# Performance work log

Hardware: AMD Instinct MI355X
Metric: run time of the kernel (lower is better)

The kernel has to match this reference:

```python
import jax, jax.numpy as jnp
import numpy as np

N = 20000      # nodes
E = 320000     # edges (before self-loops)
C_IN, C_HID, C_OUT = 256, 256, 128
NEG_SLOPE = 0.2  # PyG GATConv default


def setup_inputs() -> dict:
    key = jax.random.key(0)
    ks = jax.random.split(key, 10)
    x = jax.random.normal(ks[0], (N, C_IN), dtype=jnp.float32)
    edge_index = jax.random.randint(ks[1], (2, E), 0, N, dtype=jnp.int64)

    def glorot(k, shape, fan):
        return jax.random.normal(k, shape, dtype=jnp.float32) / np.float32(np.sqrt(fan))

    W1 = glorot(ks[2], (C_IN, C_HID), C_IN)
    a_src1 = glorot(ks[3], (C_HID,), C_HID)
    a_dst1 = glorot(ks[4], (C_HID,), C_HID)
    b1 = jnp.zeros((C_HID,), jnp.float32)
    W2 = glorot(ks[5], (C_HID, C_OUT), C_HID)
    a_src2 = glorot(ks[6], (C_OUT,), C_OUT)
    a_dst2 = glorot(ks[7], (C_OUT,), C_OUT)
    b2 = jnp.zeros((C_OUT,), jnp.float32)
    return dict(x=x, edge_index=edge_index, W1=W1, a_src1=a_src1, a_dst1=a_dst1,
                b1=b1, W2=W2, a_src2=a_src2, a_dst2=a_dst2, b2=b2)


def gat_layer(x, src, dst, W, a_src, a_dst, b, n):
    # PyG GATConv (heads=1): linear proj, additive attention, softmax over
    # incoming edges per destination node, weighted aggregation + bias.
    h = x @ W                                   # [N, F]
    alpha_src = h @ a_src                       # [N]
    alpha_dst = h @ a_dst                       # [N]
    e = jax.nn.leaky_relu(alpha_src[src] + alpha_dst[dst], NEG_SLOPE)  # [E]
    m = jax.ops.segment_max(e, dst, num_segments=n)                    # stable softmax
    e = jnp.exp(e - m[dst])
    denom = jax.ops.segment_sum(e, dst, num_segments=n)                # [N]
    out = jax.ops.segment_sum(e[:, None] * h[src], dst, num_segments=n)  # [N, F]
    return out / denom[:, None] + b


def reference(x, edge_index, W1, a_src1, a_dst1, b1, W2, a_src2, a_dst2, b2):
    n = x.shape[0]
    # GATConv adds self-loops by default
    loops = jnp.arange(n, dtype=edge_index.dtype)
    ei = jnp.concatenate([edge_index, jnp.stack([loops, loops])], axis=1)
    src, dst = ei[0], ei[1]
    h = gat_layer(x, src, dst, W1, a_src1, a_dst1, b1, n)
    h = jax.nn.relu(h)  # Dropout is identity in eval mode
    return gat_layer(h, src, dst, W2, a_src2, a_dst2, b2, n)
```

## Files before the change

### kernel.cpp

```cpp
#include <hip/hip_runtime.h>
#include <math.h>

#define N_NODES 20000
#define N_EDGES 320000
#define C_IN  256
#define C_HID 256
#define C_OUT 128
#define NEG_SLOPE 0.2f
#define CAP   256
#define GEMM1_BLKS (N_NODES / 32)
#define SCAT_BLKS  ((N_EDGES + 255) / 256)
#define AGG_PAD 280

typedef __attribute__((ext_vector_type(8))) short bf16x8;
typedef __attribute__((ext_vector_type(4))) float f32x4;

__device__ __align__(16) unsigned short c_W1h[C_IN * C_HID], c_W1l[C_IN * C_HID];
__device__ __align__(16) unsigned short c_W2h[C_HID * C_OUT], c_W2l[C_HID * C_OUT];
__device__ float c_as1f[C_HID], c_ad1f[C_HID], c_b1f[C_HID];
__device__ float c_as2f[C_OUT], c_ad2f[C_OUT], c_b2f[C_OUT];
__device__ __align__(16) unsigned short g_h1b[(size_t)N_NODES * C_HID];
__device__ __align__(16) unsigned short g_h2b[(size_t)N_NODES * C_OUT];
__device__ float g_alps1[N_NODES], g_alpd1[N_NODES];
__device__ float g_alps2[N_NODES], g_alpd2[N_NODES];
__device__ int   g_cursor[N_NODES];
__device__ int   g_srcidx[(size_t)N_NODES * CAP];
__device__ int   g_is64;
__device__ int   g_isf32;

__device__ __forceinline__ float bf2f(unsigned short b){
  unsigned int u = ((unsigned int)b) << 16;
  return __builtin_bit_cast(float, u);
}
__device__ __forceinline__ unsigned short f2bf(float f){
  unsigned int u = __builtin_bit_cast(unsigned int, f);
  u += 0x7fffu + ((u >> 16) & 1u);
  return (unsigned short)(u >> 16);
}
__device__ __forceinline__ int clampi(int v){
  v = v < 0 ? 0 : v;
  return v >= N_NODES ? N_NODES - 1 : v;
}
__device__ __forceinline__ void edge_sd(const int* ei, int e, int& s, int& d){
  if (g_is64){ s = ei[2 * e]; d = ei[2 * (N_EDGES + e)]; }
  else       { s = ei[e];     d = ei[N_EDGES + e]; }
  s = clampi(s); d = clampi(d);
}

struct Ptrs { const void* p[8]; };

__device__ __forceinline__ int wpack(int k, int n, int Nc){
  return (((k >> 5) * (Nc / 16) + (n >> 4)) * 64 + (((k >> 3) & 3) * 16 + (n & 15))) * 8 + (k & 7);
}

#define PREP_Z  N_NODES
#define PREP_W1 (C_IN * C_HID)
#define PREP_W2 (C_HID * C_OUT)
#define PREP_T  (PREP_Z + PREP_W1 + PREP_W2 + 2 * C_HID + C_HID + 2 * C_OUT + C_OUT)

__global__ void prep_k(const unsigned int* __restrict__ xw,
                       const int* __restrict__ ei, Ptrs ps){
  __shared__ int s_isf32;
  if (threadIdx.x < 64){
    int lane = (int)threadIdx.x, cnt = 0;
    for (int j = lane; j < 256; j += 64){
      unsigned int e = (xw[j] >> 7) & 0xFFu;
      if (e >= 0x60u && e <= 0x8Fu) ++cnt;
    }
#pragma unroll
    for (int o = 32; o > 0; o >>= 1) cnt += __shfl_xor(cnt, o, 64);
    if (lane == 0) s_isf32 = (cnt < 200) ? 1 : 0;
  }
  __syncthreads();
  const int isf32 = s_isf32;

  if (blockIdx.x == 0 && threadIdx.x < 64){
    unsigned long long anybad = __ballot(ei[2 * (int)threadIdx.x + 1] != 0);
    if (threadIdx.x == 0){ g_isf32 = isf32; g_is64 = (anybad == 0ULL) ? 1 : 0; }
  }

  int tid = (int)(blockIdx.x * blockDim.x + threadIdx.x);
  if (tid < PREP_Z){
    g_cursor[tid] = 0;
    g_alps1[tid] = 0.f; g_alpd1[tid] = 0.f;
    g_alps2[tid] = 0.f; g_alpd2[tid] = 0.f;
    return;
  }
  int j = tid - PREP_Z;
  auto ld = [&](const void* p, int i) -> float {
    return isf32 ? ((const float*)p)[i] : bf2f(((const unsigned short*)p)[i]);
  };
  if (j < PREP_W1){
    float f = ld(ps.p[0], j);
    int k = j / C_HID, n = j % C_HID;
    int idx = wpack(k, n, C_HID);
    unsigned short h = f2bf(f);
    c_W1h[idx] = h; c_W1l[idx] = f2bf(f - bf2f(h));
    return;
  }
  j -= PREP_W1;
  if (j < PREP_W2){
    float f = ld(ps.p[4], j);
    int k = j / C_OUT, n = j % C_OUT;
    int idx = wpack(k, n, C_OUT);
    unsigned short h = f2bf(f);
    c_W2h[idx] = h; c_W2l[idx] = f2bf(f - bf2f(h));
    return;
  }
  j -= PREP_W2;
  if      (j <  256) c_as1f[j]        = ld(ps.p[1], j);
  else if (j <  512) c_ad1f[j - 256]  = ld(ps.p[2], j - 256);
  else if (j <  768) c_b1f [j - 512]  = ld(ps.p[3], j - 512);
  else if (j <  896) c_as2f[j - 768]  = ld(ps.p[5], j - 768);
  else if (j < 1024) c_ad2f[j - 896]  = ld(ps.p[6], j - 896);
  else if (j < 1152) c_b2f [j - 1024] = ld(ps.p[7], j - 1024);
}

__global__ __launch_bounds__(256) void gemm1_k(const void* __restrict__ xsrc,
                                               const int* __restrict__ ei){
  if (blockIdx.x >= GEMM1_BLKS){
    int e = (int)(blockIdx.x - GEMM1_BLKS) * 256 + (int)threadIdx.x;
    if (e < N_EDGES){
      int s, d;
      edge_sd(ei, e, s, d);
      int pos = atomicAdd(&g_cursor[d], 1);
      if (pos < CAP) g_srcidx[(size_t)d * CAP + pos] = s;
    }
    return;
  }

  const bool isf32 = (g_isf32 != 0);
  int wid  = (int)(threadIdx.x >> 6);
  int lane = (int)(threadIdx.x & 63);
  int kgrp = lane >> 4, cl = lane & 15;
  int mbase = blockIdx.x * 32;

  f32x4 acc[2][4];
#pragma unroll
  for (int m = 0; m < 2; ++m)
#pragma unroll
    for (int n = 0; n < 4; ++n) acc[m][n] = (f32x4){0.f, 0.f, 0.f, 0.f};

  for (int kt = 0; kt < 8; ++kt){
    int kbase = kt * 32 + kgrp * 8;
    bf16x8 ah[2], al[2];
    if (isf32){
      const float* Xf = (const float*)xsrc;
#pragma unroll
      for (int m = 0; m < 2; ++m){
        const float4* xp = (const float4*)(Xf + (size_t)(mbase + m * 16 + cl) * 256 + kbase);
        float4 v0 = xp[0], v1 = xp[1];
        float vals[8] = {v0.x, v0.y, v0.z, v0.w, v1.x, v1.y, v1.z, v1.w};
#pragma unroll
        for (int j = 0; j < 8; ++j){
          unsigned short h = f2bf(vals[j]);
          ah[m][j] = (short)h;
          al[m][j] = (short)f2bf(vals[j] - bf2f(h));
        }
      }
    } else {
      const unsigned short* Xb = (const unsigned short*)xsrc;
#pragma unroll
      for (int m = 0; m < 2; ++m){
        ah[m] = *(const bf16x8*)(Xb + (size_t)(mbase + m * 16 + cl) * 256 + kbase);
        al[m] = (bf16x8){0,0,0,0,0,0,0,0};
      }
    }
#pragma unroll
    for (int nn = 0; nn < 4; ++nn){
      int nt = wid * 4 + nn;
      size_t wi = ((size_t)(kt * 16 + nt) * 64 + lane) * 8;
      bf16x8 bh = *(const bf16x8*)(c_W1h + wi);
      bf16x8 bl = *(const bf16x8*)(c_W1l + wi);
#pragma unroll
      for (int m = 0; m < 2; ++m){
        acc[m][nn] = __builtin_amdgcn_mfma_f32_16x16x32_bf16(ah[m], bh, acc[m][nn], 0, 0, 0);
        acc[m][nn] = __builtin_amdgcn_mfma_f32_16x16x32_bf16(ah[m], bl, acc[m][nn], 0, 0, 0);
        acc[m][nn] = __builtin_amdgcn_mfma_f32_16x16x32_bf16(al[m], bh, acc[m][nn], 0, 0, 0);
      }
    }
  }

  float asv[4], adv[4];
#pragma unroll
  for (int nn = 0; nn < 4; ++nn){
    int col = (wid * 4 + nn) * 16 + cl;
    asv[nn] = c_as1f[col]; adv[nn] = c_ad1f[col];
  }
#pragma unroll
  for (int m = 0; m < 2; ++m){
#pragma unroll
    for (int i = 0; i < 4; ++i){
      int row = mbase + m * 16 + kgrp * 4 + i;
      float ps = 0.f, pd = 0.f;
#pragma unroll
      for (int nn = 0; nn < 4; ++nn){
        int col = (wid * 4 + nn) * 16 + cl;
        float v = acc[m][nn][i];
        g_h1b[(size_t)row * C_HID + col] = f2bf(v);
        ps += v * asv[nn]; pd += v * adv[nn];
      }
      ps += __shfl_xor(ps, 1);  pd += __shfl_xor(pd, 1);
      ps += __shfl_xor(ps, 2);  pd += __shfl_xor(pd, 2);
      ps += __shfl_xor(ps, 4);  pd += __shfl_xor(pd, 4);
      ps += __shfl_xor(ps, 8);  pd += __shfl_xor(pd, 8);
      if (cl == 0){
        atomicAdd(&g_alps1[row], ps);
        atomicAdd(&g_alpd1[row], pd);
      }
    }
  }
}

#define ACC4(p, ww) { \
  a0 += (ww) * bf2f((unsigned short)((p).x & 0xFFFFu)); \
  a1 += (ww) * bf2f((unsigned short)((p).x >> 16)); \
  a2 += (ww) * bf2f((unsigned short)((p).y & 0xFFFFu)); \
  a3 += (ww) * bf2f((unsigned short)((p).y >> 16)); }

#define ACC2(p, ww) { \
  a0 += (ww) * bf2f((unsigned short)((p) & 0xFFFFu)); \
  a1 += (ww) * bf2f((unsigned short)((p) >> 16)); }

__global__ __launch_bounds__(256) void aggemm_k(){
  __shared__ __align__(16) unsigned short s_hi[16 * AGG_PAD];
  __shared__ __align__(16) unsigned short s_lo[16 * AGG_PAD];
  __shared__ float s_ps[4][16], s_pd[4][16];

  int lane = (int)(threadIdx.x & 63);
  int wid  = (int)(threadIdx.x >> 6);
  int nb   = blockIdx.x * 16;
  const uint2* H2 = (const uint2*)g_h1b;

  for (int q = 0; q < 4; ++q){
    int n = nb + wid * 4 + q;
    int len = g_cursor[n]; if (len > CAP) len = CAP;
    int i0 = n * CAP, i1 = i0 + len;
    float adn = g_alpd1[n];
    float dpart = 0.f;
    float a0 = 0.f, a1 = 0.f, a2 = 0.f, a3 = 0.f;

    {
      float es = g_alps1[n] + adn;
      es = (es > 0.f) ? es : NEG_SLOPE * es;
      float wself = __expf(es);
      if (lane == 0) dpart += wself;
      uint2 p = H2[(size_t)n * 64 + lane];
      ACC4(p, wself)
    }

    for (int base = i0; base < i1; base += 64){
      int nv = i1 - base; if (nv > 64) nv = 64;
      int sv = 0; float wv = 0.f;
      if (lane < nv){
        sv = g_srcidx[base + lane];
        float e = g_alps1[sv] + adn;
        e = (e > 0.f) ? e : NEG_SLOPE * e;
        wv = __expf(e);
      }
      dpart += wv;
      int j = 0;
      for (; j + 8 <= nv; j += 8){
        int s0 = __shfl(sv, j),     s1 = __shfl(sv, j + 1);
        int s2 = __shfl(sv, j + 2), s3 = __shfl(sv, j + 3);
        int s4 = __shfl(sv, j + 4), s5 = __shfl(sv, j + 5);
        int s6 = __shfl(sv, j + 6), s7 = __shfl(sv, j + 7);
        float w0 = __shfl(wv, j),     w1 = __shfl(wv, j + 1);
        float w2 = __shfl(wv, j + 2), w3 = __shfl(wv, j + 3);
        float w4 = __shfl(wv, j + 4), w5 = __shfl(wv, j + 5);
        float w6 = __shfl(wv, j + 6), w7 = __shfl(wv, j + 7);
        uint2 p0 = H2[(size_t)s0 * 64 + lane];
        uint2 p1 = H2[(size_t)s1 * 64 + lane];
        uint2 p2 = H2[(size_t)s2 * 64 + lane];
        uint2 p3 = H2[(size_t)s3 * 64 + lane];
        uint2 p4 = H2[(size_t)s4 * 64 + lane];
        uint2 p5 = H2[(size_t)s5 * 64 + lane];
        uint2 p6 = H2[(size_t)s6 * 64 + lane];
        uint2 p7 = H2[(size_t)s7 * 64 + lane];
        ACC4(p0, w0) ACC4(p1, w1) ACC4(p2, w2) ACC4(p3, w3)
        ACC4(p4, w4) ACC4(p5, w5) ACC4(p6, w6) ACC4(p7, w7)
      }
      for (; j + 4 <= nv; j += 4){
        int s0 = __shfl(sv, j),     s1 = __shfl(sv, j + 1);
        int s2 = __shfl(sv, j + 2), s3 = __shfl(sv, j + 3);
        float w0 = __shfl(wv, j),     w1 = __shfl(wv, j + 1);
        float w2 = __shfl(wv, j + 2), w3 = __shfl(wv, j + 3);
        uint2 p0 = H2[(size_t)s0 * 64 + lane];
        uint2 p1 = H2[(size_t)s1 * 64 + lane];
        uint2 p2 = H2[(size_t)s2 * 64 + lane];
        uint2 p3 = H2[(size_t)s3 * 64 + lane];
        ACC4(p0, w0) ACC4(p1, w1) ACC4(p2, w2) ACC4(p3, w3)
      }
      for (; j < nv; ++j){
        int s = __shfl(sv, j);
        float w = __shfl(wv, j);
        uint2 p = H2[(size_t)s * 64 + lane];
        ACC4(p, w)
      }
    }

    float den = dpart;
#pragma unroll
    for (int o = 32; o > 0; o >>= 1) den += __shfl_xor(den, o, 64);
    float inv = 1.f / den;

    float o0 = a0 * inv + c_b1f[4 * lane];
    float o1 = a1 * inv + c_b1f[4 * lane + 1];
    float o2 = a2 * inv + c_b1f[4 * lane + 2];
    float o3 = a3 * inv + c_b1f[4 * lane + 3];
    o0 = fmaxf(o0, 0.f); o1 = fmaxf(o1, 0.f);
    o2 = fmaxf(o2, 0.f); o3 = fmaxf(o3, 0.f);
    unsigned short h0 = f2bf(o0), h1 = f2bf(o1), h2 = f2bf(o2), h3 = f2bf(o3);
    uint2 ph, pl;
    ph.x = (unsigned)h0 | ((unsigned)h1 << 16);
    ph.y = (unsigned)h2 | ((unsigned)h3 << 16);
    pl.x = (unsigned)f2bf(o0 - bf2f(h0)) | ((unsigned)f2bf(o1 - bf2f(h1)) << 16);
    pl.y = (unsigned)f2bf(o2 - bf2f(h2)) | ((unsigned)f2bf(o3 - bf2f(h3)) << 16);
    int r = wid * 4 + q;
    *(uint2*)&s_hi[r * AGG_PAD + 4 * lane] = ph;
    *(uint2*)&s_lo[r * AGG_PAD + 4 * lane] = pl;
  }
  __syncthreads();

  int kgrp = lane >> 4, cl = lane & 15;
  f32x4 acc[2];
  acc[0] = (f32x4){0.f, 0.f, 0.f, 0.f};
  acc[1] = (f32x4){0.f, 0.f, 0.f, 0.f};
  for (int kt = 0; kt < 8; ++kt){
    int rb = cl * AGG_PAD + kt * 32 + kgrp * 8;
    bf16x8 ah = *(const bf16x8*)&s_hi[rb];
    bf16x8 al = *(const bf16x8*)&s_lo[rb];
#pragma unroll
    for (int nn = 0; nn < 2; ++nn){
      int nt = wid * 2 + nn;
      size_t wi = ((size_t)(kt * 8 + nt) * 64 + lane) * 8;
      bf16x8 bh = *(const bf16x8*)(c_W2h + wi);
      bf16x8 bl = *(const bf16x8*)(c_W2l + wi);
      acc[nn] = __builtin_amdgcn_mfma_f32_16x16x32_bf16(ah, bh, acc[nn], 0, 0, 0);
      acc[nn] = __builtin_amdgcn_mfma_f32_16x16x32_bf16(ah, bl, acc[nn], 0, 0, 0);
      acc[nn] = __builtin_amdgcn_mfma_f32_16x16x32_bf16(al, bh, acc[nn], 0, 0, 0);
    }
  }

  float asv[2], adv[2];
#pragma unroll
  for (int nn = 0; nn < 2; ++nn){
    int col = (wid * 2 + nn) * 16 + cl;
    asv[nn] = c_as2f[col]; adv[nn] = c_ad2f[col];
  }
#pragma unroll
  for (int i = 0; i < 4; ++i){
    int row = nb + kgrp * 4 + i;
    float ps = 0.f, pd = 0.f;
#pragma unroll
    for (int nn = 0; nn < 2; ++nn){
      int col = (wid * 2 + nn) * 16 + cl;
      float v = acc[nn][i];
      g_h2b[(size_t)row * C_OUT + col] = f2bf(v);
      ps += v * asv[nn]; pd += v * adv[nn];
    }
    ps += __shfl_xor(ps, 1);  pd += __shfl_xor(pd, 1);
    ps += __shfl_xor(ps, 2);  pd += __shfl_xor(pd, 2);
    ps += __shfl_xor(ps, 4);  pd += __shfl_xor(pd, 4);
    ps += __shfl_xor(ps, 8);  pd += __shfl_xor(pd, 8);
    if (cl == 0){ s_ps[wid][kgrp * 4 + i] = ps; s_pd[wid][kgrp * 4 + i] = pd; }
  }
  __syncthreads();
  if (threadIdx.x < 16){
    int r = (int)threadIdx.x;
    g_alps2[nb + r] = s_ps[0][r] + s_ps[1][r] + s_ps[2][r] + s_ps[3][r];
    g_alpd2[nb + r] = s_pd[0][r] + s_pd[1][r] + s_pd[2][r] + s_pd[3][r];
  }
}

__global__ void agg2_k(float* OUT){
  int lane = (int)(threadIdx.x & 63);
  int n = blockIdx.x * 4 + (int)(threadIdx.x >> 6);
  int len = g_cursor[n]; if (len > CAP) len = CAP;
  int i0 = n * CAP, i1 = i0 + len;
  float adn = g_alpd2[n];
  float dpart = 0.f;
  float a0 = 0.f, a1 = 0.f;
  const unsigned int* H1 = (const unsigned int*)g_h2b;

  {
    float es = g_alps2[n] + adn;
    es = (es > 0.f) ? es : NEG_SLOPE * es;
    float wself = __expf(es);
    if (lane == 0) dpart += wself;
    unsigned int p = H1[(size_t)n * 64 + lane];
    ACC2(p, wself)
  }

  for (int base = i0; base < i1; base += 64){
    int nv = i1 - base; if (nv > 64) nv = 64;
    int sv = 0; float wv = 0.f;
    if (lane < nv){
      sv = g_srcidx[base + lane];
      float e = g_alps2[sv] + adn;
      e = (e > 0.f) ? e : NEG_SLOPE * e;
      wv = __expf(e);
    }
    dpart += wv;
    int j = 0;
    for (; j + 8 <= nv; j += 8){
      int s0 = __shfl(sv, j),     s1 = __shfl(sv, j + 1);
      int s2 = __shfl(sv, j + 2), s3 = __shfl(sv, j + 3);
      int s4 = __shfl(sv, j + 4), s5 = __shfl(sv, j + 5);
      int s6 = __shfl(sv, j + 6), s7 = __shfl(sv, j + 7);
      float w0 = __shfl(wv, j),     w1 = __shfl(wv, j + 1);
      float w2 = __shfl(wv, j + 2), w3 = __shfl(wv, j + 3);
      float w4 = __shfl(wv, j + 4), w5 = __shfl(wv, j + 5);
      float w6 = __shfl(wv, j + 6), w7 = __shfl(wv, j + 7);
      unsigned int p0 = H1[(size_t)s0 * 64 + lane];
      unsigned int p1 = H1[(size_t)s1 * 64 + lane];
      unsigned int p2 = H1[(size_t)s2 * 64 + lane];
      unsigned int p3 = H1[(size_t)s3 * 64 + lane];
      unsigned int p4 = H1[(size_t)s4 * 64 + lane];
      unsigned int p5 = H1[(size_t)s5 * 64 + lane];
      unsigned int p6 = H1[(size_t)s6 * 64 + lane];
      unsigned int p7 = H1[(size_t)s7 * 64 + lane];
      ACC2(p0, w0) ACC2(p1, w1) ACC2(p2, w2) ACC2(p3, w3)
      ACC2(p4, w4) ACC2(p5, w5) ACC2(p6, w6) ACC2(p7, w7)
    }
    for (; j + 4 <= nv; j += 4){
      int s0 = __shfl(sv, j),     s1 = __shfl(sv, j + 1);
      int s2 = __shfl(sv, j + 2), s3 = __shfl(sv, j + 3);
      float w0 = __shfl(wv, j),     w1 = __shfl(wv, j + 1);
      float w2 = __shfl(wv, j + 2), w3 = __shfl(wv, j + 3);
      unsigned int p0 = H1[(size_t)s0 * 64 + lane];
      unsigned int p1 = H1[(size_t)s1 * 64 + lane];
      unsigned int p2 = H1[(size_t)s2 * 64 + lane];
      unsigned int p3 = H1[(size_t)s3 * 64 + lane];
      ACC2(p0, w0) ACC2(p1, w1) ACC2(p2, w2) ACC2(p3, w3)
    }
    for (; j < nv; ++j){
      int s = __shfl(sv, j);
      float w = __shfl(wv, j);
      unsigned int p = H1[(size_t)s * 64 + lane];
      ACC2(p, w)
    }
  }

  float den = dpart;
#pragma unroll
  for (int o = 32; o > 0; o >>= 1) den += __shfl_xor(den, o, 64);
  float inv = 1.f / den;

  float2 o;
  o.x = a0 * inv + c_b2f[2 * lane];
  o.y = a1 * inv + c_b2f[2 * lane + 1];
  ((float2*)OUT)[(size_t)n * 64 + lane] = o;
}

extern "C" void kernel_launch(void* const* d_in, const int* in_sizes, int n_in,
                              void* d_out, int out_size, void* d_ws, size_t ws_size,
                              hipStream_t stream){
  (void)in_sizes; (void)n_in; (void)out_size; (void)d_ws; (void)ws_size;
  const void* x  = d_in[0];
  const int*  ei = (const int*)d_in[1];
  float* out = (float*)d_out;

  Ptrs ps;
  ps.p[0] = d_in[2]; ps.p[1] = d_in[3]; ps.p[2] = d_in[4]; ps.p[3] = d_in[5];
  ps.p[4] = d_in[6]; ps.p[5] = d_in[7]; ps.p[6] = d_in[8]; ps.p[7] = d_in[9];

  prep_k<<<(PREP_T + 255) / 256, 256, 0, stream>>>((const unsigned int*)x, ei, ps);

  gemm1_k<<<GEMM1_BLKS + SCAT_BLKS, 256, 0, stream>>>(x, ei);

  aggemm_k<<<N_NODES / 16, 256, 0, stream>>>();

  agg2_k<<<N_NODES / 4, 256, 0, stream>>>(out);
}
```

Before: 165.6 us.

## Process two nodes per wavefront with wider gathers; replace alpha atomics with LDS reduction

Both aggregation kernels now split each 64-lane wavefront into two 32-lane halves, each handling a different destination node, and each lane gathers 16-byte (layer 1) or 8-byte (layer 2) rows instead of 8 or 4 bytes. The aim is fewer, wider memory transactions and more nodes in flight per wave. The cost is that both halves loop to the larger of the two neighbour counts, so lanes sit idle when degrees differ. In the first GEMM, the per-row attention dot products are now reduced across waves in shared memory and stored directly, instead of being accumulated with global atomics. That also removes the zero-initialisation of the alpha arrays in the prep kernel.

```diff
diff --git a/kernel.cpp b/kernel.cpp
--- a/kernel.cpp
+++ b/kernel.cpp
@@ -82,8 +82,6 @@
   int tid = (int)(blockIdx.x * blockDim.x + threadIdx.x);
   if (tid < PREP_Z){
     g_cursor[tid] = 0;
-    g_alps1[tid] = 0.f; g_alpd1[tid] = 0.f;
-    g_alps2[tid] = 0.f; g_alpd2[tid] = 0.f;
     return;
   }
   int j = tid - PREP_Z;
@@ -129,6 +127,8 @@
     return;
   }
 
+  __shared__ float s_ps[4][32], s_pd[4][32];
+
   const bool isf32 = (g_isf32 != 0);
   int wid  = (int)(threadIdx.x >> 6);
   int lane = (int)(threadIdx.x & 63);
@@ -191,7 +191,8 @@
   for (int m = 0; m < 2; ++m){
 #pragma unroll
     for (int i = 0; i < 4; ++i){
-      int row = mbase + m * 16 + kgrp * 4 + i;
+      int rl = m * 16 + kgrp * 4 + i;
+      int row = mbase + rl;
       float ps = 0.f, pd = 0.f;
 #pragma unroll
       for (int nn = 0; nn < 4; ++nn){
@@ -204,13 +205,26 @@
       ps += __shfl_xor(ps, 2);  pd += __shfl_xor(pd, 2);
       ps += __shfl_xor(ps, 4);  pd += __shfl_xor(pd, 4);
       ps += __shfl_xor(ps, 8);  pd += __shfl_xor(pd, 8);
-      if (cl == 0){
-        atomicAdd(&g_alps1[row], ps);
-        atomicAdd(&g_alpd1[row], pd);
-      }
-    }
-  }
-}
+      if (cl == 0){ s_ps[wid][rl] = ps; s_pd[wid][rl] = pd; }
+    }
+  }
+  __syncthreads();
+  if (threadIdx.x < 32){
+    int r = (int)threadIdx.x;
+    g_alps1[mbase + r] = s_ps[0][r] + s_ps[1][r] + s_ps[2][r] + s_ps[3][r];
+    g_alpd1[mbase + r] = s_pd[0][r] + s_pd[1][r] + s_pd[2][r] + s_pd[3][r];
+  }
+}
+
+#define ACC8(p, ww) { \
+  a0 += (ww) * bf2f((unsigned short)((p).x & 0xFFFFu)); \
+  a1 += (ww) * bf2f((unsigned short)((p).x >> 16)); \
+  a2 += (ww) * bf2f((unsigned short)((p).y & 0xFFFFu)); \
+  a3 += (ww) * bf2f((unsigned short)((p).y >> 16)); \
+  a4 += (ww) * bf2f((unsigned short)((p).z & 0xFFFFu)); \
+  a5 += (ww) * bf2f((unsigned short)((p).z >> 16)); \
+  a6 += (ww) * bf2f((unsigned short)((p).w & 0xFFFFu)); \
+  a7 += (ww) * bf2f((unsigned short)((p).w >> 16)); }
 
 #define ACC4(p, ww) { \
   a0 += (ww) * bf2f((unsigned short)((p).x & 0xFFFFu)); \
@@ -218,10 +232,6 @@
   a2 += (ww) * bf2f((unsigned short)((p).y & 0xFFFFu)); \
   a3 += (ww) * bf2f((unsigned short)((p).y >> 16)); }
 
-#define ACC2(p, ww) { \
-  a0 += (ww) * bf2f((unsigned short)((p) & 0xFFFFu)); \
-  a1 += (ww) * bf2f((unsigned short)((p) >> 16)); }
-
 __global__ __launch_bounds__(256) void aggemm_k(){
   __shared__ __align__(16) unsigned short s_hi[16 * AGG_PAD];
   __shared__ __align__(16) unsigned short s_lo[16 * AGG_PAD];
@@ -229,96 +239,90 @@
 
   int lane = (int)(threadIdx.x & 63);
   int wid  = (int)(threadIdx.x >> 6);
+  int hl   = lane & 31;
+  int half = lane >> 5;
   int nb   = blockIdx.x * 16;
-  const uint2* H2 = (const uint2*)g_h1b;
-
-  for (int q = 0; q < 4; ++q){
-    int n = nb + wid * 4 + q;
+  const uint4* H4 = (const uint4*)g_h1b;
+
+  for (int q = 0; q < 2; ++q){
+    int n = nb + wid * 4 + 2 * q + half;
     int len = g_cursor[n]; if (len > CAP) len = CAP;
-    int i0 = n * CAP, i1 = i0 + len;
+    int lenmax; { int lo = __shfl_xor(len, 32); lenmax = lo > len ? lo : len; }
     float adn = g_alpd1[n];
-    float dpart = 0.f;
     float a0 = 0.f, a1 = 0.f, a2 = 0.f, a3 = 0.f;
-
+    float a4 = 0.f, a5 = 0.f, a6 = 0.f, a7 = 0.f;
+
+    float es = g_alps1[n] + adn;
+    es = (es > 0.f) ? es : NEG_SLOPE * es;
+    float wself = __expf(es);
+    float dpart = (hl == 0) ? wself : 0.f;
     {
-      float es = g_alps1[n] + adn;
-      es = (es > 0.f) ? es : NEG_SLOPE * es;
-      float wself = __expf(es);
-      if (lane == 0) dpart += wself;
-      uint2 p = H2[(size_t)n * 64 + lane];
-      ACC4(p, wself)
-    }
-
-    for (int base = i0; base < i1; base += 64){
-      int nv = i1 - base; if (nv > 64) nv = 64;
-      int sv = 0; float wv = 0.f;
-      if (lane < nv){
-        sv = g_srcidx[base + lane];
+      uint4 p = H4[(size_t)n * 32 + hl];
+      ACC8(p, wself)
+    }
+
+    for (int base = 0; base < lenmax; base += 32){
+      int rem = len - base;
+      int nv = rem < 0 ? 0 : (rem > 32 ? 32 : rem);
+      int remx = lenmax - base;
+      int nvmax = remx > 32 ? 32 : remx;
+      int sv = n; float wv = 0.f;
+      if (hl < nv){
+        sv = g_srcidx[(size_t)n * CAP + base + hl];
         float e = g_alps1[sv] + adn;
         e = (e > 0.f) ? e : NEG_SLOPE * e;
         wv = __expf(e);
       }
       dpart += wv;
       int j = 0;
-      for (; j + 8 <= nv; j += 8){
-        int s0 = __shfl(sv, j),     s1 = __shfl(sv, j + 1);
-        int s2 = __shfl(sv, j + 2), s3 = __shfl(sv, j + 3);
-        int s4 = __shfl(sv, j + 4), s5 = __shfl(sv, j + 5);
-        int s6 = __shfl(sv, j + 6), s7 = __shfl(sv, j + 7);
-        float w0 = __shfl(wv, j),     w1 = __shfl(wv, j + 1);
-        float w2 = __shfl(wv, j + 2), w3 = __shfl(wv, j + 3);
-        float w4 = __shfl(wv, j + 4), w5 = __shfl(wv, j + 5);
-        float w6 = __shfl(wv, j + 6), w7 = __shfl(wv, j + 7);
-        uint2 p0 = H2[(size_t)s0 * 64 + lane];
-        uint2 p1 = H2[(size_t)s1 * 64 + lane];
-        uint2 p2 = H2[(size_t)s2 * 64 + lane];
-        uint2 p3 = H2[(size_t)s3 * 64 + lane];
-        uint2 p4 = H2[(size_t)s4 * 64 + lane];
-        uint2 p5 = H2[(size_t)s5 * 64 + lane];
-        uint2 p6 = H2[(size_t)s6 * 64 + lane];
-        uint2 p7 = H2[(size_t)s7 * 64 + lane];
-        ACC4(p0, w0) ACC4(p1, w1) ACC4(p2, w2) ACC4(p3, w3)
-        ACC4(p4, w4) ACC4(p5, w5) ACC4(p6, w6) ACC4(p7, w7)
-      }
-      for (; j + 4 <= nv; j += 4){
-        int s0 = __shfl(sv, j),     s1 = __shfl(sv, j + 1);
-        int s2 = __shfl(sv, j + 2), s3 = __shfl(sv, j + 3);
-        float w0 = __shfl(wv, j),     w1 = __shfl(wv, j + 1);
-        float w2 = __shfl(wv, j + 2), w3 = __shfl(wv, j + 3);
-        uint2 p0 = H2[(size_t)s0 * 64 + lane];
-        uint2 p1 = H2[(size_t)s1 * 64 + lane];
-        uint2 p2 = H2[(size_t)s2 * 64 + lane];
-        uint2 p3 = H2[(size_t)s3 * 64 + lane];
-        ACC4(p0, w0) ACC4(p1, w1) ACC4(p2, w2) ACC4(p3, w3)
-      }
-      for (; j < nv; ++j){
-        int s = __shfl(sv, j);
-        float w = __shfl(wv, j);
-        uint2 p = H2[(size_t)s * 64 + lane];
-        ACC4(p, w)
+      for (; j + 4 <= nvmax; j += 4){
+        int s0 = __shfl(sv, j, 32),     s1 = __shfl(sv, j + 1, 32);
+        int s2 = __shfl(sv, j + 2, 32), s3 = __shfl(sv, j + 3, 32);
+        float w0 = __shfl(wv, j, 32),     w1 = __shfl(wv, j + 1, 32);
+        float w2 = __shfl(wv, j + 2, 32), w3 = __shfl(wv, j + 3, 32);
+        uint4 p0 = H4[(size_t)s0 * 32 + hl];
+        uint4 p1 = H4[(size_t)s1 * 32 + hl];
+        uint4 p2 = H4[(size_t)s2 * 32 + hl];
+        uint4 p3 = H4[(size_t)s3 * 32 + hl];
+        ACC8(p0, w0) ACC8(p1, w1) ACC8(p2, w2) ACC8(p3, w3)
+      }
+      for (; j < nvmax; ++j){
+        int s = __shfl(sv, j, 32);
+        float w = __shfl(wv, j, 32);
+        uint4 p = H4[(size_t)s * 32 + hl];
+        ACC8(p, w)
       }
     }
 
     float den = dpart;
 #pragma unroll
-    for (int o = 32; o > 0; o >>= 1) den += __shfl_xor(den, o, 64);
+    for (int o = 16; o > 0; o >>= 1) den += __shfl_xor(den, o, 32);
     float inv = 1.f / den;
 
-    float o0 = a0 * inv + c_b1f[4 * lane];
-    float o1 = a1 * inv + c_b1f[4 * lane + 1];
-    float o2 = a2 * inv + c_b1f[4 * lane + 2];
-    float o3 = a3 * inv + c_b1f[4 * lane + 3];
-    o0 = fmaxf(o0, 0.f); o1 = fmaxf(o1, 0.f);
-    o2 = fmaxf(o2, 0.f); o3 = fmaxf(o3, 0.f);
+    float o0 = a0 * inv + c_b1f[8 * hl];
+    float o1 = a1 * inv + c_b1f[8 * hl + 1];
+    float o2 = a2 * inv + c_b1f[8 * hl + 2];
+    float o3 = a3 * inv + c_b1f[8 * hl + 3];
+    float o4 = a4 * inv + c_b1f[8 * hl + 4];
+    float o5 = a5 * inv + c_b1f[8 * hl + 5];
+    float o6 = a6 * inv + c_b1f[8 * hl + 6];
+    float o7 = a7 * inv + c_b1f[8 * hl + 7];
+    o0 = fmaxf(o0, 0.f); o1 = fmaxf(o1, 0.f); o2 = fmaxf(o2, 0.f); o3 = fmaxf(o3, 0.f);
+    o4 = fmaxf(o4, 0.f); o5 = fmaxf(o5, 0.f); o6 = fmaxf(o6, 0.f); o7 = fmaxf(o7, 0.f);
     unsigned short h0 = f2bf(o0), h1 = f2bf(o1), h2 = f2bf(o2), h3 = f2bf(o3);
-    uint2 ph, pl;
+    unsigned short h4 = f2bf(o4), h5 = f2bf(o5), h6 = f2bf(o6), h7 = f2bf(o7);
+    uint4 ph, pl;
     ph.x = (unsigned)h0 | ((unsigned)h1 << 16);
     ph.y = (unsigned)h2 | ((unsigned)h3 << 16);
+    ph.z = (unsigned)h4 | ((unsigned)h5 << 16);
+    ph.w = (unsigned)h6 | ((unsigned)h7 << 16);
     pl.x = (unsigned)f2bf(o0 - bf2f(h0)) | ((unsigned)f2bf(o1 - bf2f(h1)) << 16);
     pl.y = (unsigned)f2bf(o2 - bf2f(h2)) | ((unsigned)f2bf(o3 - bf2f(h3)) << 16);
-    int r = wid * 4 + q;
-    *(uint2*)&s_hi[r * AGG_PAD + 4 * lane] = ph;
-    *(uint2*)&s_lo[r * AGG_PAD + 4 * lane] = pl;
+    pl.z = (unsigned)f2bf(o4 - bf2f(h4)) | ((unsigned)f2bf(o5 - bf2f(h5)) << 16);
+    pl.w = (unsigned)f2bf(o6 - bf2f(h6)) | ((unsigned)f2bf(o7 - bf2f(h7)) << 16);
+    int r = wid * 4 + 2 * q + half;
+    *(uint4*)&s_hi[r * AGG_PAD + 8 * hl] = ph;
+    *(uint4*)&s_lo[r * AGG_PAD + 8 * hl] = pl;
   }
   __syncthreads();
 
@@ -373,84 +377,92 @@
   }
 }
 
-__global__ void agg2_k(float* OUT){
+__global__ __launch_bounds__(256) void agg2_k(float* OUT){
   int lane = (int)(threadIdx.x & 63);
-  int n = blockIdx.x * 4 + (int)(threadIdx.x >> 6);
+  int wid  = (int)(threadIdx.x >> 6);
+  int hl   = lane & 31;
+  int half = lane >> 5;
+  int n = blockIdx.x * 8 + wid * 2 + half;
+  const uint2* H2 = (const uint2*)g_h2b;
+
   int len = g_cursor[n]; if (len > CAP) len = CAP;
-  int i0 = n * CAP, i1 = i0 + len;
+  int lenmax; { int lo = __shfl_xor(len, 32); lenmax = lo > len ? lo : len; }
   float adn = g_alpd2[n];
-  float dpart = 0.f;
-  float a0 = 0.f, a1 = 0.f;
-  const unsigned int* H1 = (const unsigned int*)g_h2b;
-
+  float a0 = 0.f, a1 = 0.f, a2 = 0.f, a3 = 0.f;
+
+  float es = g_alps2[n] + adn;
+  es = (es > 0.f) ? es : NEG_SLOPE * es;
+  float wself = __expf(es);
+  float dpart = (hl == 0) ? wself : 0.f;
   {
-    float es = g_alps2[n] + adn;
-    es = (es > 0.f) ? es : NEG_SLOPE * es;
-    float wself = __expf(es);
-    if (lane == 0) dpart += wself;
-    unsigned int p = H1[(size_t)n * 64 + lane];
-    ACC2(p, wself)
-  }
-
-  for (int base = i0; base < i1; base += 64){
-    int nv = i1 - base; if (nv > 64) nv = 64;
-    int sv = 0; float wv = 0.f;
-    if (lane < nv){
-      sv = g_srcidx[base + lane];
+    uint2 p = H2[(size_t)n * 32 + hl];
+    ACC4(p, wself)
+  }
+
+  for (int base = 0; base < lenmax; base += 32){
+    int rem = len - base;
+    int nv = rem < 0 ? 0 : (rem > 32 ? 32 : rem);
+    int remx = lenmax - base;
+    int nvmax = remx > 32 ? 32 : remx;
+    int sv = n; float wv = 0.f;
+    if (hl < nv){
+      sv = g_srcidx[(size_t)n * CAP + base + hl];
       float e = g_alps2[sv] + adn;
       e = (e > 0.f) ? e : NEG_SLOPE * e;
       wv = __expf(e);
     }
     dpart += wv;
     int j = 0;
-    for (; j + 8 <= nv; j += 8){
-      int s0 = __shfl(sv, j),     s1 = __shfl(sv, j + 1);
-      int s2 = __shfl(sv, j + 2), s3 = __shfl(sv, j + 3);
-      int s4 = __shfl(sv, j + 4), s5 = __shfl(sv, j + 5);
-      int s6 = __shfl(sv, j + 6), s7 = __shfl(sv, j + 7);
-      float w0 = __shfl(wv, j),     w1 = __shfl(wv, j + 1);
-      float w2 = __shfl(wv, j + 2), w3 = __shfl(wv, j + 3);
-      float w4 = __shfl(wv, j + 4), w5 = __shfl(wv, j + 5);
-      float w6 = __shfl(wv, j + 6), w7 = __shfl(wv, j + 7);
-      unsigned int p0 = H1[(size_t)s0 * 64 + lane];
-      unsigned int p1 = H1[(size_t)s1 * 64 + lane];
-      unsigned int p2 = H1[(size_t)s2 * 64 + lane];
-      unsigned int p3 = H1[(size_t)s3 * 64 + lane];
-      unsigned int p4 = H1[(size_t)s4 * 64 + lane];
-      unsigned int p5 = H1[(size_t)s5 * 64 + lane];
-      unsigned int p6 = H1[(size_t)s6 * 64 + lane];
-      unsigned int p7 = H1[(size_t)s7 * 64 + lane];
-      ACC2(p0, w0) ACC2(p1, w1) ACC2(p2, w2) ACC2(p3, w3)
-      ACC2(p4, w4) ACC2(p5, w5) ACC2(p6, w6) ACC2(p7, w7)
-    }
-    for (; j + 4 <= nv; j += 4){
-      int s0 = __shfl(sv, j),     s1 = __shfl(sv, j + 1);
-      int s2 = __shfl(sv, j + 2), s3 = __shfl(sv, j + 3);
-      float w0 = __shfl(wv, j),     w1 = __shfl(wv, j + 1);
-      float w2 = __shfl(wv, j + 2), w3 = __shfl(wv, j + 3);
-      unsigned int p0 = H1[(size_t)s0 * 64 + lane];
-      unsigned int p1 = H1[(size_t)s1 * 64 + lane];
-      unsigned int p2 = H1[(size_t)s2 * 64 + lane];
-      unsigned int p3 = H1[(size_t)s3 * 64 + lane];
-      ACC2(p0, w0) ACC2(p1, w1) ACC2(p2, w2) ACC2(p3, w3)
-    }
-    for (; j < nv; ++j){
-      int s = __shfl(sv, j);
-      float w = __shfl(wv, j);
-      unsigned int p = H1[(size_t)s * 64 + lane];
-      ACC2(p, w)
+    for (; j + 8 <= nvmax; j += 8){
+      int s0 = __shfl(sv, j, 32),     s1 = __shfl(sv, j + 1, 32);
+      int s2 = __shfl(sv, j + 2, 32), s3 = __shfl(sv, j + 3, 32);
+      int s4 = __shfl(sv, j + 4, 32), s5 = __shfl(sv, j + 5, 32);
+      int s6 = __shfl(sv, j + 6, 32), s7 = __shfl(sv, j + 7, 32);
+      float w0 = __shfl(wv, j, 32),     w1 = __shfl(wv, j + 1, 32);
+      float w2 = __shfl(wv, j + 2, 32), w3 = __shfl(wv, j + 3, 32);
+      float w4 = __shfl(wv, j + 4, 32), w5 = __shfl(wv, j + 5, 32);
+      float w6 = __shfl(wv, j + 6, 32), w7 = __shfl(wv, j + 7, 32);
+      uint2 p0 = H2[(size_t)s0 * 32 + hl];
+      uint2 p1 = H2[(size_t)s1 * 32 + hl];
+      uint2 p2 = H2[(size_t)s2 * 32 + hl];
+      uint2 p3 = H2[(size_t)s3 * 32 + hl];
+      uint2 p4 = H2[(size_t)s4 * 32 + hl];
+      uint2 p5 = H2[(size_t)s5 * 32 + hl];
+      uint2 p6 = H2[(size_t)s6 * 32 + hl];
+      uint2 p7 = H2[(size_t)s7 * 32 + hl];
+      ACC4(p0, w0) ACC4(p1, w1) ACC4(p2, w2) ACC4(p3, w3)
+      ACC4(p4, w4) ACC4(p5, w5) ACC4(p6, w6) ACC4(p7, w7)
+    }
+    for (; j + 4 <= nvmax; j += 4){
+      int s0 = __shfl(sv, j, 32),     s1 = __shfl(sv, j + 1, 32);
+      int s2 = __shfl(sv, j + 2, 32), s3 = __shfl(sv, j + 3, 32);
+      float w0 = __shfl(wv, j, 32),     w1 = __shfl(wv, j + 1, 32);
+      float w2 = __shfl(wv, j + 2, 32), w3 = __shfl(wv, j + 3, 32);
+      uint2 p0 = H2[(size_t)s0 * 32 + hl];
+      uint2 p1 = H2[(size_t)s1 * 32 + hl];
+      uint2 p2 = H2[(size_t)s2 * 32 + hl];
+      uint2 p3 = H2[(size_t)s3 * 32 + hl];
+      ACC4(p0, w0) ACC4(p1, w1) ACC4(p2, w2) ACC4(p3, w3)
+    }
+    for (; j < nvmax; ++j){
+      int s = __shfl(sv, j, 32);
+      float w = __shfl(wv, j, 32);
+      uint2 p = H2[(size_t)s * 32 + hl];
+      ACC4(p, w)
     }
   }
 
   float den = dpart;
 #pragma unroll
-  for (int o = 32; o > 0; o >>= 1) den += __shfl_xor(den, o, 64);
+  for (int o = 16; o > 0; o >>= 1) den += __shfl_xor(den, o, 32);
   float inv = 1.f / den;
 
-  float2 o;
-  o.x = a0 * inv + c_b2f[2 * lane];
-  o.y = a1 * inv + c_b2f[2 * lane + 1];
-  ((float2*)OUT)[(size_t)n * 64 + lane] = o;
+  float4 o;
+  o.x = a0 * inv + c_b2f[4 * hl];
+  o.y = a1 * inv + c_b2f[4 * hl + 1];
+  o.z = a2 * inv + c_b2f[4 * hl + 2];
+  o.w = a3 * inv + c_b2f[4 * hl + 3];
+  ((float4*)OUT)[(size_t)n * 32 + hl] = o;
 }
 
 extern "C" void kernel_launch(void* const* d_in, const int* in_sizes, int n_in,
@@ -471,5 +483,5 @@
 
   aggemm_k<<<N_NODES / 16, 256, 0, stream>>>();
 
-  agg2_k<<<N_NODES / 4, 256, 0, stream>>>(out);
-}
+  agg2_k<<<N_NODES / 8, 256, 0, stream>>>(out);
+}
```

After: 170.7 us. +3.1%, slower.
